# Kernel tuning notes

Hardware: AMD Instinct MI355X
Metric: run time of the kernel (lower is better)

## Reference

```python
import jax, jax.numpy as jnp
import numpy as np

B, T, D = 2048, 200, 64
H1, H2 = 80, 40  # att_hidden_units


def setup_inputs() -> dict:
    key = jax.random.key(0)
    ks = jax.random.split(key, 11)
    inp = {
        "q": jax.random.normal(ks[0], (B, D), dtype=jnp.float32),
        "k": jax.random.normal(ks[1], (B, T, D), dtype=jnp.float32),
        "v": jax.random.normal(ks[2], (B, T, D), dtype=jnp.float32),
        # Dense 1: in = 4*D (concat of q,k,q-k,q*k)
        "W1": jax.random.normal(ks[3], (4 * D, H1), dtype=jnp.float32) * (1.0 / np.sqrt(4 * D)),
        "b1": jnp.zeros((H1,), dtype=jnp.float32),
        # PReLU alpha, keras default shape = input_shape[1:] = (T, H1)
        "a1": jax.random.uniform(ks[4], (T, H1), dtype=jnp.float32) * 0.25,
        "W2": jax.random.normal(ks[5], (H1, H2), dtype=jnp.float32) * (1.0 / np.sqrt(H1)),
        "b2": jnp.zeros((H2,), dtype=jnp.float32),
        "a2": jax.random.uniform(ks[6], (T, H2), dtype=jnp.float32) * 0.25,
        # final Dense(1)
        "Wf": jax.random.normal(ks[7], (H2, 1), dtype=jnp.float32) * (1.0 / np.sqrt(H2)),
        "bf": jnp.zeros((1,), dtype=jnp.float32),
    }
    return inp


def _prelu(x, alpha):
    return jnp.where(x > 0, x, alpha * x)


def reference(q, k, v, W1, b1, a1, W2, b2, a2, Wf, bf):
    Bb, Tt, Dd = k.shape
    # tf.tile + reshape == broadcast q over the history/time axis
    qe = jnp.broadcast_to(q[:, None, :], (Bb, Tt, Dd))  # [B, T, D]
    info = jnp.concatenate([qe, k, qe - k, qe * k], axis=-1)  # [B, T, 4D]
    h = _prelu(jnp.einsum('bti,ij->btj', info, W1) + b1, a1)   # [B, T, H1]
    h = _prelu(jnp.einsum('bti,ij->btj', h, W2) + b2, a2)      # [B, T, H2]
    logits = (jnp.einsum('bti,ij->btj', h, Wf) + bf)[..., 0]    # [B, T]
    w = jax.nn.softmax(logits, axis=-1)                          # [B, T]
    return jnp.einsum('bt,btd->bd', w, v)                        # [B, D]
```

## Files before the change

kernel.cpp:

```cpp
#include <hip/hip_runtime.h>
#include <math.h>

#define B_  2048
#define T_  200

typedef short short8 __attribute__((ext_vector_type(8)));
typedef float f32x4  __attribute__((ext_vector_type(4)));

__device__ __forceinline__ unsigned short f2bf_rne(float x) {
    unsigned u = __float_as_uint(x);
    unsigned r = u + 0x7FFFu + ((u >> 16) & 1u);
    return (unsigned short)(r >> 16);
}
__device__ __forceinline__ float bf2f(unsigned short h) {
    return __uint_as_float(((unsigned)h) << 16);
}
__device__ __forceinline__ void split2(float x, unsigned short& hi, unsigned short& lo) {
    hi = f2bf_rne(x); lo = f2bf_rne(x - bf2f(hi));
}

__global__ __launch_bounds__(256, 3)
void att_kernel(const float* __restrict__ q,
                const float* __restrict__ k,
                const float* __restrict__ v,
                const float* __restrict__ W1,
                const float* __restrict__ b1,
                const float* __restrict__ a1,
                const float* __restrict__ W2,
                const float* __restrict__ b2,
                const float* __restrict__ a2,
                const float* __restrict__ Wf,
                const float* __restrict__ bf,
                float* __restrict__ out)
{
    const int b    = blockIdx.x;
    const int tid  = threadIdx.x;
    const int lane = tid & 63;
    const int wv   = __builtin_amdgcn_readfirstlane(tid >> 6);
    const int ncl  = lane & 15;
    const int q4   = lane >> 4;
    const int kq   = q4 * 8;

    __shared__ unsigned short s_wqhi[80 * 72];
    __shared__ unsigned short s_wqlo[80 * 72];
    __shared__ __align__(16) unsigned short s_h1[2 * 64 * 104];
    __shared__ float s_q[64];
    __shared__ float s_base1[80];
    __shared__ float s_logits[256];

    unsigned short* s_h1hi = s_h1;
    unsigned short* s_h1lo = s_h1 + 64 * 104;
    float*  u_w   = (float*)s_h1;
    float4* u_acc = (float4*)(s_h1 + 512);
    float*  u_red = (float*)(s_h1 + 2560);

    const float* kb = k + (size_t)b * T_ * 64;
    const float* vb = v + (size_t)b * T_ * 64;

    if (tid < 64) s_q[tid] = q[b * 64 + tid];
    __syncthreads();

    for (int idx = tid; idx < 5120; idx += 256) {
        const int kk = idx / 80, j = idx - kk * 80;
        const float x = W1[5120 + idx] - W1[10240 + idx] + s_q[kk] * W1[15360 + idx];
        unsigned short hi, lo; split2(x, hi, lo);
        s_wqhi[j * 72 + kk] = hi;
        s_wqlo[j * 72 + kk] = lo;
    }
    if (tid < 80) {
        float s0 = b1[tid], s1 = 0.f;
        #pragma unroll 4
        for (int i = 0; i < 64; i += 2) {
            s0 += s_q[i]     * (W1[i * 80 + tid]       + W1[10240 + i * 80 + tid]);
            s1 += s_q[i + 1] * (W1[(i + 1) * 80 + tid] + W1[10240 + (i + 1) * 80 + tid]);
        }
        s_base1[tid] = s0 + s1;
    }
    for (int idx = tid; idx < 1024; idx += 256) {
        const int r = idx >> 4, c = 80 + (idx & 15);
        s_h1hi[r * 104 + c] = 0;
        s_h1lo[r * 104 + c] = 0;
    }
    __syncthreads();

    short8 w2h[3][3], w2l[3][3];
    #pragma unroll
    for (int nt = 0; nt < 3; ++nt) {
        const int n = nt * 16 + ncl;
        #pragma unroll
        for (int c = 0; c < 3; ++c) {
            short8 hh, ll;
            #pragma unroll
            for (int jj = 0; jj < 8; ++jj) {
                const int kk = c * 32 + kq + jj;
                const float x = (kk < 80 && n < 40) ? W2[kk * 40 + n] : 0.f;
                unsigned short hi, lo; split2(x, hi, lo);
                hh[jj] = (short)hi; ll[jj] = (short)lo;
            }
            w2h[nt][c] = hh; w2l[nt][c] = ll;
        }
    }
    float wf3[3], b23[3], bb1[5];
    #pragma unroll
    for (int nt = 0; nt < 3; ++nt) {
        const int n = nt * 16 + ncl;
        wf3[nt] = (n < 40) ? Wf[n] : 0.f;
        b23[nt] = (n < 40) ? b2[n] : 0.f;
    }
    #pragma unroll
    for (int nt = 0; nt < 5; ++nt) bb1[nt] = s_base1[nt * 16 + ncl];
    const float bfv = bf[0];

    const int h1row = (wv * 16 + ncl) * 104;
    for (int mt = wv; mt < 13; mt += 4) {
        const int trow = mt * 16 + ncl;
        float4 ka0 = {0,0,0,0}, ka1 = ka0, ka2 = ka0, ka3 = ka0;
        if (trow < T_) {
            const float4* kr = (const float4*)(kb + trow * 64);
            ka0 = kr[q4 * 2];     ka1 = kr[q4 * 2 + 1];
            ka2 = kr[8 + q4 * 2]; ka3 = kr[8 + q4 * 2 + 1];
        }
        const float a0v[8] = {ka0.x, ka0.y, ka0.z, ka0.w, ka1.x, ka1.y, ka1.z, ka1.w};
        const float a1v[8] = {ka2.x, ka2.y, ka2.z, ka2.w, ka3.x, ka3.y, ka3.z, ka3.w};
        short8 ahi0, alo0, ahi1, alo1;
        #pragma unroll
        for (int jj = 0; jj < 8; ++jj) {
            unsigned short h, l;
            split2(a0v[jj], h, l); ahi0[jj] = (short)h; alo0[jj] = (short)l;
            split2(a1v[jj], h, l); ahi1[jj] = (short)h; alo1[jj] = (short)l;
        }

        #pragma unroll
        for (int nt = 0; nt < 5; ++nt) {
            const int n = nt * 16 + ncl;
            const short8 bhi0 = *(const short8*)&s_wqhi[n * 72 + kq];
            const short8 bhi1 = *(const short8*)&s_wqhi[n * 72 + 32 + kq];
            const short8 blo0 = *(const short8*)&s_wqlo[n * 72 + kq];
            const short8 blo1 = *(const short8*)&s_wqlo[n * 72 + 32 + kq];
            f32x4 acc = {0.f, 0.f, 0.f, 0.f};
            acc = __builtin_amdgcn_mfma_f32_16x16x32_bf16(ahi0, blo0, acc, 0, 0, 0);
            acc = __builtin_amdgcn_mfma_f32_16x16x32_bf16(alo0, bhi0, acc, 0, 0, 0);
            acc = __builtin_amdgcn_mfma_f32_16x16x32_bf16(ahi1, blo1, acc, 0, 0, 0);
            acc = __builtin_amdgcn_mfma_f32_16x16x32_bf16(alo1, bhi1, acc, 0, 0, 0);
            acc = __builtin_amdgcn_mfma_f32_16x16x32_bf16(ahi0, bhi0, acc, 0, 0, 0);
            acc = __builtin_amdgcn_mfma_f32_16x16x32_bf16(ahi1, bhi1, acc, 0, 0, 0);
            #pragma unroll
            for (int r = 0; r < 4; ++r) {
                const int rloc = q4 * 4 + r;
                int t = mt * 16 + rloc; if (t > T_ - 1) t = T_ - 1;
                float x = acc[r] + bb1[nt];
                const float al = a1[t * 80 + n];
                x = x > 0.f ? x : al * x;
                unsigned short hi, lo; split2(x, hi, lo);
                s_h1hi[(wv * 16 + rloc) * 104 + n] = hi;
                s_h1lo[(wv * 16 + rloc) * 104 + n] = lo;
            }
        }

        short8 ah[3], al[3];
        #pragma unroll
        for (int c = 0; c < 3; ++c) {
            ah[c] = *(const short8*)&s_h1hi[h1row + c * 32 + kq];
            al[c] = *(const short8*)&s_h1lo[h1row + c * 32 + kq];
        }
        float part[4] = {0.f, 0.f, 0.f, 0.f};
        #pragma unroll
        for (int nt = 0; nt < 3; ++nt) {
            f32x4 acc = {0.f, 0.f, 0.f, 0.f};
            #pragma unroll
            for (int c = 0; c < 3; ++c) {
                acc = __builtin_amdgcn_mfma_f32_16x16x32_bf16(ah[c], w2l[nt][c], acc, 0, 0, 0);
                acc = __builtin_amdgcn_mfma_f32_16x16x32_bf16(al[c], w2h[nt][c], acc, 0, 0, 0);
                acc = __builtin_amdgcn_mfma_f32_16x16x32_bf16(ah[c], w2h[nt][c], acc, 0, 0, 0);
            }
            const int n = nt * 16 + ncl;
            #pragma unroll
            for (int r = 0; r < 4; ++r) {
                int t = mt * 16 + q4 * 4 + r; if (t > T_ - 1) t = T_ - 1;
                float x = acc[r] + b23[nt];
                const float al2 = (n < 40) ? a2[t * 40 + n] : 0.f;
                x = x > 0.f ? x : al2 * x;
                part[r] += x * wf3[nt];
            }
        }
        #pragma unroll
        for (int r = 0; r < 4; ++r) {
            float p = part[r];
            p += __shfl_xor(p, 1, 64);
            p += __shfl_xor(p, 2, 64);
            p += __shfl_xor(p, 4, 64);
            p += __shfl_xor(p, 8, 64);
            part[r] = p;
        }
        if (ncl == 0) {
            #pragma unroll
            for (int r = 0; r < 4; ++r) {
                const int t = mt * 16 + q4 * 4 + r;
                if (t < T_) s_logits[t] = part[r] + bfv;
            }
        }
    }
    __syncthreads();

    float logit = -INFINITY;
    if (tid < T_) logit = s_logits[tid];
    float mred = logit;
    #pragma unroll
    for (int off = 1; off < 64; off <<= 1) mred = fmaxf(mred, __shfl_xor(mred, off, 64));
    if (lane == 0) u_red[wv] = mred;
    __syncthreads();
    const float mx = fmaxf(fmaxf(u_red[0], u_red[1]), fmaxf(u_red[2], u_red[3]));
    const float ew = (tid < T_) ? __expf(logit - mx) : 0.f;
    float ssum = ew;
    #pragma unroll
    for (int off = 1; off < 64; off <<= 1) ssum += __shfl_xor(ssum, off, 64);
    if (lane == 0) u_red[4 + wv] = ssum;
    __syncthreads();
    const float tot = (u_red[4] + u_red[5]) + (u_red[6] + u_red[7]);
    const float inv = 1.0f / tot;
    u_w[tid] = ew * inv;
    __syncthreads();

    const int c4 = tid & 15, g = tid >> 4;
    float4 acc4 = {0.f, 0.f, 0.f, 0.f};
    const float4* vb4 = (const float4*)vb;
    for (int t = g; t < T_; t += 16) {
        const float wt = u_w[t];
        const float4 vv = vb4[t * 16 + c4];
        acc4.x += wt * vv.x; acc4.y += wt * vv.y;
        acc4.z += wt * vv.z; acc4.w += wt * vv.w;
    }
    u_acc[tid] = acc4;
    __syncthreads();
    if (tid < 64) {
        const float* uf = (const float*)u_acc;
        float s = 0.f;
        #pragma unroll
        for (int gg = 0; gg < 16; ++gg) s += uf[gg * 64 + tid];
        out[b * 64 + tid] = s;
    }
}

extern "C" void kernel_launch(void* const* d_in, const int* in_sizes, int n_in,
                              void* d_out, int out_size, void* d_ws, size_t ws_size,
                              hipStream_t stream) {
    const float* q  = (const float*)d_in[0];
    const float* k  = (const float*)d_in[1];
    const float* v  = (const float*)d_in[2];
    const float* W1 = (const float*)d_in[3];
    const float* b1 = (const float*)d_in[4];
    const float* a1 = (const float*)d_in[5];
    const float* W2 = (const float*)d_in[6];
    const float* b2 = (const float*)d_in[7];
    const float* a2 = (const float*)d_in[8];
    const float* Wf = (const float*)d_in[9];
    const float* bf = (const float*)d_in[10];
    float* out = (float*)d_out;

    hipLaunchKernelGGL(att_kernel, dim3(B_), dim3(256), 0, stream,
                       q, k, v, W1, b1, a1, W2, b2, a2, Wf, bf, out);
}
```

Before: 344.0 us.

## Prefetch k, PReLU alphas and v into registers to overlap global loads

Issues the first k tile and the a1/a2 alpha loads before the W1 preprocessing, then software-pipelines the next tile's k and alpha loads during the current tile's MFMA work. The v rows are loaded into registers before the softmax so that latency overlaps the reductions. The q-bias dot product is also split across 240 threads in three partial sums. The intent is to hide global-memory latency, at the cost of many more live registers under launch_bounds(256,3), which risks spills or lower occupancy.

New measurement: 486.3 us. +41.4%, slower.

```diff
diff --git a/kernel.cpp b/kernel.cpp
--- a/kernel.cpp
+++ b/kernel.cpp
@@ -45,7 +45,7 @@
     __shared__ unsigned short s_wqlo[80 * 72];
     __shared__ __align__(16) unsigned short s_h1[2 * 64 * 104];
     __shared__ float s_q[64];
-    __shared__ float s_base1[80];
+    __shared__ float s_b1p[240];
     __shared__ float s_logits[256];
 
     unsigned short* s_h1hi = s_h1;
@@ -56,6 +56,33 @@
 
     const float* kb = k + (size_t)b * T_ * 64;
     const float* vb = v + (size_t)b * T_ * 64;
+
+    float4 pk0, pk1, pk2, pk3;
+    float  pa1[5][4];
+    float  pa2[3][4];
+    {
+        const int trow = wv * 16 + ncl;
+        const float4* kr = (const float4*)(kb + trow * 64);
+        pk0 = kr[q4 * 2];     pk1 = kr[q4 * 2 + 1];
+        pk2 = kr[8 + q4 * 2]; pk3 = kr[8 + q4 * 2 + 1];
+        #pragma unroll
+        for (int nt = 0; nt < 5; ++nt) {
+            #pragma unroll
+            for (int r = 0; r < 4; ++r) {
+                const int t = wv * 16 + q4 * 4 + r;
+                pa1[nt][r] = a1[t * 80 + nt * 16 + ncl];
+            }
+        }
+        #pragma unroll
+        for (int nt = 0; nt < 3; ++nt) {
+            const int n2 = nt * 16 + ncl;
+            #pragma unroll
+            for (int r = 0; r < 4; ++r) {
+                const int t = wv * 16 + q4 * 4 + r;
+                pa2[nt][r] = (n2 < 40) ? a2[t * 40 + n2] : 0.f;
+            }
+        }
+    }
 
     if (tid < 64) s_q[tid] = q[b * 64 + tid];
     __syncthreads();
@@ -67,14 +94,15 @@
         s_wqhi[j * 72 + kk] = hi;
         s_wqlo[j * 72 + kk] = lo;
     }
-    if (tid < 80) {
-        float s0 = b1[tid], s1 = 0.f;
-        #pragma unroll 4
-        for (int i = 0; i < 64; i += 2) {
-            s0 += s_q[i]     * (W1[i * 80 + tid]       + W1[10240 + i * 80 + tid]);
-            s1 += s_q[i + 1] * (W1[(i + 1) * 80 + tid] + W1[10240 + (i + 1) * 80 + tid]);
-        }
-        s_base1[tid] = s0 + s1;
+    if (tid < 240) {
+        const int part = tid / 80;
+        const int j    = tid - part * 80;
+        const int k0   = (part == 0) ? 0  : (part == 1 ? 22 : 43);
+        const int k1   = (part == 0) ? 22 : (part == 1 ? 43 : 64);
+        float s = 0.f;
+        for (int i = k0; i < k1; ++i)
+            s += s_q[i] * (W1[i * 80 + j] + W1[10240 + i * 80 + j]);
+        s_b1p[tid] = s;
     }
     for (int idx = tid; idx < 1024; idx += 256) {
         const int r = idx >> 4, c = 80 + (idx & 15);
@@ -108,26 +136,35 @@
         b23[nt] = (n < 40) ? b2[n] : 0.f;
     }
     #pragma unroll
-    for (int nt = 0; nt < 5; ++nt) bb1[nt] = s_base1[nt * 16 + ncl];
+    for (int nt = 0; nt < 5; ++nt) {
+        const int n = nt * 16 + ncl;
+        bb1[nt] = b1[n] + s_b1p[n] + s_b1p[80 + n] + s_b1p[160 + n];
+    }
     const float bfv = bf[0];
 
     const int h1row = (wv * 16 + ncl) * 104;
     for (int mt = wv; mt < 13; mt += 4) {
-        const int trow = mt * 16 + ncl;
-        float4 ka0 = {0,0,0,0}, ka1 = ka0, ka2 = ka0, ka3 = ka0;
-        if (trow < T_) {
-            const float4* kr = (const float4*)(kb + trow * 64);
-            ka0 = kr[q4 * 2];     ka1 = kr[q4 * 2 + 1];
-            ka2 = kr[8 + q4 * 2]; ka3 = kr[8 + q4 * 2 + 1];
-        }
-        const float a0v[8] = {ka0.x, ka0.y, ka0.z, ka0.w, ka1.x, ka1.y, ka1.z, ka1.w};
-        const float a1v[8] = {ka2.x, ka2.y, ka2.z, ka2.w, ka3.x, ka3.y, ka3.z, ka3.w};
+        const float a0v[8] = {pk0.x, pk0.y, pk0.z, pk0.w, pk1.x, pk1.y, pk1.z, pk1.w};
+        const float a1v[8] = {pk2.x, pk2.y, pk2.z, pk2.w, pk3.x, pk3.y, pk3.z, pk3.w};
         short8 ahi0, alo0, ahi1, alo1;
         #pragma unroll
         for (int jj = 0; jj < 8; ++jj) {
             unsigned short h, l;
             split2(a0v[jj], h, l); ahi0[jj] = (short)h; alo0[jj] = (short)l;
             split2(a1v[jj], h, l); ahi1[jj] = (short)h; alo1[jj] = (short)l;
+        }
+
+        const int mtn = mt + 4;
+        if (mtn < 13) {
+            const int trow = mtn * 16 + ncl;
+            if (trow < T_) {
+                const float4* kr = (const float4*)(kb + trow * 64);
+                pk0 = kr[q4 * 2];     pk1 = kr[q4 * 2 + 1];
+                pk2 = kr[8 + q4 * 2]; pk3 = kr[8 + q4 * 2 + 1];
+            } else {
+                pk0 = make_float4(0.f, 0.f, 0.f, 0.f);
+                pk1 = pk0; pk2 = pk0; pk3 = pk0;
+            }
         }
 
         #pragma unroll
@@ -147,9 +184,8 @@
             #pragma unroll
             for (int r = 0; r < 4; ++r) {
                 const int rloc = q4 * 4 + r;
-                int t = mt * 16 + rloc; if (t > T_ - 1) t = T_ - 1;
                 float x = acc[r] + bb1[nt];
-                const float al = a1[t * 80 + n];
+                const float al = pa1[nt][r];
                 x = x > 0.f ? x : al * x;
                 unsigned short hi, lo; split2(x, hi, lo);
                 s_h1hi[(wv * 16 + rloc) * 104 + n] = hi;
@@ -173,12 +209,10 @@
                 acc = __builtin_amdgcn_mfma_f32_16x16x32_bf16(al[c], w2h[nt][c], acc, 0, 0, 0);
                 acc = __builtin_amdgcn_mfma_f32_16x16x32_bf16(ah[c], w2h[nt][c], acc, 0, 0, 0);
             }
-            const int n = nt * 16 + ncl;
-            #pragma unroll
-            for (int r = 0; r < 4; ++r) {
-                int t = mt * 16 + q4 * 4 + r; if (t > T_ - 1) t = T_ - 1;
+            #pragma unroll
+            for (int r = 0; r < 4; ++r) {
                 float x = acc[r] + b23[nt];
-                const float al2 = (n < 40) ? a2[t * 40 + n] : 0.f;
+                const float al2 = pa2[nt][r];
                 x = x > 0.f ? x : al2 * x;
                 part[r] += x * wf3[nt];
             }
@@ -199,8 +233,37 @@
                 if (t < T_) s_logits[t] = part[r] + bfv;
             }
         }
-    }
-    __syncthreads();
+
+        if (mtn < 13) {
+            #pragma unroll
+            for (int nt = 0; nt < 5; ++nt) {
+                #pragma unroll
+                for (int r = 0; r < 4; ++r) {
+                    int t = mtn * 16 + q4 * 4 + r; if (t > T_ - 1) t = T_ - 1;
+                    pa1[nt][r] = a1[t * 80 + nt * 16 + ncl];
+                }
+            }
+            #pragma unroll
+            for (int nt = 0; nt < 3; ++nt) {
+                const int n2 = nt * 16 + ncl;
+                #pragma unroll
+                for (int r = 0; r < 4; ++r) {
+                    int t = mtn * 16 + q4 * 4 + r; if (t > T_ - 1) t = T_ - 1;
+                    pa2[nt][r] = (n2 < 40) ? a2[t * 40 + n2] : 0.f;
+                }
+            }
+        }
+    }
+    __syncthreads();
+
+    const int c4 = tid & 15, g = tid >> 4;
+    const float4* vb4 = (const float4*)vb;
+    float4 pv[13];
+    #pragma unroll
+    for (int i = 0; i < 13; ++i) {
+        int t = g + i * 16; if (t > T_ - 1) t = T_ - 1;
+        pv[i] = vb4[t * 16 + c4];
+    }
 
     float logit = -INFINITY;
     if (tid < T_) logit = s_logits[tid];
@@ -221,14 +284,13 @@
     u_w[tid] = ew * inv;
     __syncthreads();
 
-    const int c4 = tid & 15, g = tid >> 4;
     float4 acc4 = {0.f, 0.f, 0.f, 0.f};
-    const float4* vb4 = (const float4*)vb;
-    for (int t = g; t < T_; t += 16) {
-        const float wt = u_w[t];
-        const float4 vv = vb4[t * 16 + c4];
-        acc4.x += wt * vv.x; acc4.y += wt * vv.y;
-        acc4.z += wt * vv.z; acc4.w += wt * vv.w;
+    #pragma unroll
+    for (int i = 0; i < 13; ++i) {
+        const int t = g + i * 16;
+        const float wt = (t < T_) ? u_w[t] : 0.f;
+        acc4.x += wt * pv[i].x; acc4.y += wt * pv[i].y;
+        acc4.z += wt * pv[i].z; acc4.w += wt * pv[i].w;
     }
     u_acc[tid] = acc4;
     __syncthreads();
```
